# Kernel tuning notes

Measured on AMD Instinct MI355X. Metric: run time of the kernel, lower is better.

The kernel has to match this reference:

```python
import jax, jax.numpy as jnp
import numpy as np

BN_EPS = 1e-5
NEG = -9e15
ALPHA = 0.2  # LeakyReLU slope


def _gat(src, tgt, adj_mask, W, a, num_heads):
    # src: [M, H*D] source features, tgt: [N, H*D], adj_mask: [N, M] (>0 means edge)
    N, M = tgt.shape[0], src.shape[0]
    D = tgt.shape[1] // num_heads
    S = (src @ W.T).reshape(M, num_heads, D)   # W(source)
    T = (tgt @ W.T).reshape(N, num_heads, D)   # W(target)
    # concat([t_i, s_j]) . a[h] == t_i . a[h,:D] + s_j . a[h,D:]
    et = jnp.einsum('nhd,hd->hn', T, a[:, :D])  # [H, N]
    es = jnp.einsum('mhd,hd->hm', S, a[:, D:])  # [H, M]
    e = et[:, :, None] + es[:, None, :]          # [H, N, M]
    e = jnp.where(e >= 0, e, ALPHA * e)          # LeakyReLU
    e = jnp.where(adj_mask[None, :, :] > 0, e, NEG)
    attn = jax.nn.softmax(e, axis=-1)            # over source nodes
    out = jnp.einsum('hnm,mhd->nhd', attn, S)    # [N, H, D]
    return out.reshape(N, num_heads * D)


def _bn_eval(x, gamma, beta):
    # eval-mode BatchNorm1d with running_mean=0, running_var=1
    return x * (gamma / jnp.sqrt(1.0 + BN_EPS)) + beta


def setup_inputs() -> dict:
    key = jax.random.key(0)
    ks = jax.random.split(key, 12)
    N, M, H, HD = 4096, 2048, 8, 256
    D = HD // H
    c_features = jax.random.normal(ks[0], (N, HD), dtype=jnp.float32)
    d_features = jax.random.normal(ks[1], (M, HD), dtype=jnp.float32)
    cd_adj = jax.random.randint(ks[2], (N, M), 0, 2, dtype=jnp.int32)
    sc = 1.0 / np.sqrt(HD)
    c_W = jax.random.normal(ks[3], (HD, HD), dtype=jnp.float32) * sc
    d_W = jax.random.normal(ks[4], (HD, HD), dtype=jnp.float32) * sc
    sa = np.sqrt(2.0 / (H + 2 * D))  # xavier_normal_ for [H, 2D]
    c_a = jax.random.normal(ks[5], (H, 2 * D), dtype=jnp.float32) * sa
    d_a = jax.random.normal(ks[6], (H, 2 * D), dtype=jnp.float32) * sa
    c_bn_gamma = jnp.ones((HD,), dtype=jnp.float32)
    c_bn_beta = jnp.zeros((HD,), dtype=jnp.float32)
    d_bn_gamma = jnp.ones((HD,), dtype=jnp.float32)
    d_bn_beta = jnp.zeros((HD,), dtype=jnp.float32)
    return dict(c_features=c_features, d_features=d_features, cd_adj=cd_adj,
                c_W=c_W, c_a=c_a, d_W=d_W, d_a=d_a,
                c_bn_gamma=c_bn_gamma, c_bn_beta=c_bn_beta,
                d_bn_gamma=d_bn_gamma, d_bn_beta=d_bn_beta)


def reference(c_features, d_features, cd_adj, c_W, c_a, d_W, d_a,
              c_bn_gamma, c_bn_beta, d_bn_gamma, d_bn_beta):
    H = 8
    c_out = _gat(d_features, c_features, cd_adj, c_W, c_a, H)
    d_out = _gat(c_features, d_features, cd_adj.T, d_W, d_a, H)
    c_out = jax.nn.relu(_bn_eval(c_out, c_bn_gamma, c_bn_beta))
    d_out = jax.nn.relu(_bn_eval(d_out, d_bn_gamma, d_bn_beta))
    # dropout is identity in eval mode
    return (c_out, d_out)
```

## Files before the change

### kernel.cpp

```cpp
#include <hip/hip_runtime.h>
#include <hip/hip_bf16.h>

#define L2E 1.4426950408889634f
#define BNF 0.99999500003749969f

typedef __attribute__((ext_vector_type(4))) float f4;
typedef __attribute__((ext_vector_type(4))) float f32x4;
typedef __attribute__((ext_vector_type(4))) int i4;
typedef __attribute__((ext_vector_type(8))) short bfrag;

__device__ __forceinline__ int cvtpk(float lo, float hi) {
  int r;
  asm("v_cvt_pk_bf16_f32 %0, %1, %2" : "=v"(r) : "v"(lo), "v"(hi));
  return r;
}

#define MFMA16(a, b, c) __builtin_amdgcn_mfma_f32_16x16x32_bf16(a, b, c, 0, 0, 0)

__global__ __launch_bounds__(256) void prep1(
    const float* __restrict__ c_feat, const float* __restrict__ d_feat,
    const float* __restrict__ c_W, const float* __restrict__ d_W,
    const float* __restrict__ c_a, const float* __restrict__ d_a,
    const int* __restrict__ adj,
    unsigned* __restrict__ adjP, unsigned* __restrict__ adjPT,
    unsigned short* __restrict__ Xb_c, unsigned short* __restrict__ Xb_d,
    unsigned short* __restrict__ Wb_c, unsigned short* __restrict__ Wb_d,
    float* __restrict__ wa_c, float* __restrict__ wa_d) {
  const int b = blockIdx.x;
  const int t = threadIdx.x;
  if (b < 2048) {
    __shared__ int s[64][65];
    const int m0 = (b & 31) * 64, n0 = (b >> 5) * 64;
#pragma unroll
    for (int i = 0; i < 4; ++i) {
      int idx = t + i * 256;
      int r = idx >> 4, c4 = (idx & 15) * 4;
      i4 v = __builtin_nontemporal_load(
          (const i4*)(adj + (size_t)(n0 + r) * 2048 + m0 + c4));
      s[r][c4 + 0] = v.x; s[r][c4 + 1] = v.y;
      s[r][c4 + 2] = v.z; s[r][c4 + 3] = v.w;
    }
    __syncthreads();
    const int w = t >> 6, l = t & 63;
#pragma unroll 4
    for (int rr = 0; rr < 16; ++rr) {
      int r = w * 16 + rr;
      int n = n0 + r;
      unsigned long long bb = __ballot(s[r][l] != 0);
      if (l == 0) {
        size_t base = ((size_t)(n >> 4) * 64 + (m0 >> 5)) * 16 + (n & 15);
        adjP[base] = (unsigned)bb;
        adjP[base + 16] = (unsigned)(bb >> 32);
      }
    }
#pragma unroll 4
    for (int cc = 0; cc < 16; ++cc) {
      int m = m0 + w * 16 + cc;
      unsigned long long bb = __ballot(s[l][w * 16 + cc] != 0);
      if (l == 0) {
        size_t base = ((size_t)(m >> 4) * 128 + (n0 >> 5)) * 16 + (m & 15);
        adjPT[base] = (unsigned)bb;
        adjPT[base + 16] = (unsigned)(bb >> 32);
      }
    }
  } else if (b < 2880) {
    int idx = (b - 2048) * 256 + t;
    const float* S; unsigned short* D; int tt;
    if (idx < 65536)       { S = d_feat; D = Xb_c; tt = idx; }
    else if (idx < 196608) { S = c_feat; D = Xb_d; tt = idx - 65536; }
    else if (idx < 204800) { S = c_W;    D = Wb_c; tt = idx - 196608; }
    else                   { S = d_W;    D = Wb_d; tt = idx - 204800; }
    int l = tt & 63, kt = (tt >> 6) & 7, tile = tt >> 9;
    int row = tile * 16 + (l & 15);
    int col = kt * 32 + (l >> 4) * 8;
    const float* sp = S + (size_t)row * 256 + col;
    f4 v0 = *(const f4*)sp;
    f4 v1 = *(const f4*)(sp + 4);
    uint4 u;
    u.x = (unsigned)cvtpk(v0.x, v0.y);
    u.y = (unsigned)cvtpk(v0.z, v0.w);
    u.z = (unsigned)cvtpk(v1.x, v1.y);
    u.w = (unsigned)cvtpk(v1.z, v1.w);
    *(uint4*)(D + (size_t)tt * 8) = u;
  } else {
    int idx = (b - 2880) * 256 + t;
    bool cs = idx < 2048;
    int i2 = idx & 2047;
    int h = i2 >> 8, k = i2 & 255;
    const float* W = cs ? c_W : d_W;
    const float* a = cs ? c_a : d_a;
    float s = 0.f;
#pragma unroll 8
    for (int d = 0; d < 32; ++d)
      s = fmaf(a[h * 64 + d], W[(size_t)(h * 32 + d) * 256 + k], s);
    (cs ? wa_c : wa_d)[i2] = s * L2E;
  }
}

__global__ __launch_bounds__(64) void gemm2(
    const unsigned short* __restrict__ Xb_c, const unsigned short* __restrict__ Wb_c,
    const unsigned short* __restrict__ Xb_d, const unsigned short* __restrict__ Wb_d,
    const float* __restrict__ c_a, const float* __restrict__ d_a,
    unsigned short* __restrict__ Sbt_c, unsigned short* __restrict__ Sbt_d,
    float* __restrict__ es2t_c, float* __restrict__ es2t_d,
    const float* __restrict__ c_feat, const float* __restrict__ d_feat,
    const float* __restrict__ wa_c, const float* __restrict__ wa_d,
    float* __restrict__ et2_c, float* __restrict__ et2_d) {
  const int b = blockIdx.x;
  if (b < 768) {
    const bool cs = b < 256;
    const int bb = cs ? b : b - 256;
    const int rt = bb >> 1, half = bb & 1;
    const unsigned short* Xb = cs ? Xb_c : Xb_d;
    const unsigned short* Wb = cs ? Wb_c : Wb_d;
    const float* av = cs ? c_a : d_a;
    unsigned short* Sbt = cs ? Sbt_c : Sbt_d;
    float* es2t = cs ? es2t_c : es2t_d;
    const int Mrows = cs ? 2048 : 4096;
    const int l = threadIdx.x;
    const int g = l >> 4, c16 = l & 15;
    bfrag afr[8];
#pragma unroll
    for (int kt = 0; kt < 8; ++kt)
      afr[kt] = *(const bfrag*)(Xb + ((size_t)(rt * 8 + kt) * 64 + l) * 8);
    float esacc[4] = {};
#pragma unroll
    for (int c8 = 0; c8 < 8; ++c8) {
      const int cht = half * 8 + c8;
      f32x4 acc = {0.f, 0.f, 0.f, 0.f};
#pragma unroll
      for (int kt = 0; kt < 8; ++kt) {
        bfrag wfr = *(const bfrag*)(Wb + ((size_t)(cht * 8 + kt) * 64 + l) * 8);
        acc = MFMA16(afr[kt], wfr, acc);
      }
      const int mtb = rt * 2 + (g >> 1);
      size_t soff = (((size_t)cht * (Mrows >> 3) + mtb) * 16 + c16) * 8 + (g & 1) * 4;
      uint2 u;
      u.x = (unsigned)cvtpk(acc[0], acc[1]);
      u.y = (unsigned)cvtpk(acc[2], acc[3]);
      *(uint2*)(Sbt + soff) = u;
      const int h = cht >> 1, sub = cht & 1;
      const float aw = av[h * 64 + 32 + sub * 16 + c16];
      if (sub == 0) {
#pragma unroll
        for (int i = 0; i < 4; ++i) esacc[i] = acc[i] * aw;
      } else {
#pragma unroll
        for (int i = 0; i < 4; ++i) esacc[i] = fmaf(acc[i], aw, esacc[i]);
#pragma unroll
        for (int i = 0; i < 4; ++i) {
          esacc[i] += __shfl_xor(esacc[i], 1);
          esacc[i] += __shfl_xor(esacc[i], 2);
          esacc[i] += __shfl_xor(esacc[i], 4);
          esacc[i] += __shfl_xor(esacc[i], 8);
        }
        if (c16 == 0) {
          f4 o = {esacc[0] * L2E, esacc[1] * L2E, esacc[2] * L2E, esacc[3] * L2E};
          *(f4*)(es2t + (size_t)h * Mrows + rt * 16 + g * 4) = o;
        }
      }
    }
  } else {
    int idx = (b - 768) * 64 + threadIdx.x;
    bool cs = idx < 32768;
    int i2 = cs ? idx : idx - 32768;
    const float* X = cs ? c_feat : d_feat;
    const float* wa = cs ? wa_c : wa_d;
    float* et2 = cs ? et2_c : et2_d;
    int r = i2 >> 3, h = i2 & 7;
    const float* xp = X + (size_t)r * 256;
    const float* ap = wa + h * 256;
    float s = 0.f;
#pragma unroll 16
    for (int k = 0; k < 256; k += 4) {
      f4 xv = *(const f4*)(xp + k);
      f4 av = *(const f4*)(ap + k);
      s = fmaf(xv.x, av.x, s); s = fmaf(xv.y, av.y, s);
      s = fmaf(xv.z, av.z, s); s = fmaf(xv.w, av.w, s);
    }
    et2[i2] = s;
  }
}

__device__ __forceinline__ bfrag make_pfrag2(float et, f4 e0, f4 e1,
                                             unsigned bits) {
  float xv[8] = {e0.x, e0.y, e0.z, e0.w, e1.x, e1.y, e1.z, e1.w};
  float p[8];
#pragma unroll
  for (int e = 0; e < 8; ++e) {
    float x = et + xv[e];
    x = fmaxf(x, 0.2f * x);
    float pe = __builtin_amdgcn_exp2f(x);
    p[e] = ((bits >> e) & 1u) ? pe : 0.f;
  }
  union { bfrag v; int i[4]; } u;
#pragma unroll
  for (int e = 0; e < 4; ++e) u.i[e] = cvtpk(p[2 * e], p[2 * e + 1]);
  return u.v;
}

template <int FINAL, int SWZ, int CHT>
__global__ __launch_bounds__(256) void fused_attn(
    const float* __restrict__ et2_c, const float* __restrict__ es2t_c,
    const unsigned* __restrict__ adjP, const unsigned short* __restrict__ Sbt_c,
    float* __restrict__ pnum_c, float* __restrict__ pden_c,
    const float* __restrict__ et2_d, const float* __restrict__ es2t_d,
    const unsigned* __restrict__ adjPT, const unsigned short* __restrict__ Sbt_d,
    float* __restrict__ pnum_d, float* __restrict__ pden_d,
    float* __restrict__ out,
    const float* __restrict__ gc, const float* __restrict__ bc,
    const float* __restrict__ gd, const float* __restrict__ bd,
    int NBC, int CH_C, int CH_D) {
  const int b = blockIdx.x;
  bool cs; int chunk, tile;
  if (SWZ) {
    const int r = b & 7;
    if (r < 4) { cs = true;  chunk = r >> 1; tile = (b >> 3) + (r & 1) * 128; }
    else       { cs = false; chunk = r - 4;  tile = b >> 3; }
  } else {
    cs = b < NBC;
    const int bb = cs ? b : b - NBC;
    tile = cs ? (bb & 255) : (bb & 127);
    chunk = cs ? (bb >> 8) : (bb >> 7);
  }
  const int n0 = tile * 16;
  const int M = cs ? 2048 : 4096;
  const int ROWS = cs ? 4096 : 2048;
  const int CH = CHT ? CHT : (cs ? CH_C : CH_D);
  const float* et2 = cs ? et2_c : et2_d;
  const float* es2t = cs ? es2t_c : es2t_d;
  const unsigned* adjPk = cs ? adjP : adjPT;
  const unsigned short* Sbt = cs ? Sbt_c : Sbt_d;
  float* pnum = cs ? pnum_c : pnum_d;
  float* pden = cs ? pden_c : pden_d;
  const float* bng = cs ? gc : gd;
  const float* bnb = cs ? bc : bd;
  float* outp = cs ? out : out + (size_t)4096 * 256;

  const int mstart = chunk * CH;
  const int mend = mstart + CH;
  const int Mw = M >> 5;
  const int tid = threadIdx.x;
  const int w = tid >> 6, l = tid & 63;
  const int g = l >> 4, c16 = l & 15;
  const int hA = w * 2, hB = w * 2 + 1;
  const int row = n0 + c16;
  const float etA = et2[row * 8 + hA];
  const float etB = et2[row * 8 + hB];
  const int Mt16 = M * 16;
  const int lane_off = g * 128 + c16 * 8;
  const unsigned short* pA0 = Sbt + (size_t)(hA * 2) * Mt16 + lane_off;
  const unsigned short* pA1 = pA0 + Mt16;
  const unsigned short* pB0 = Sbt + (size_t)(hB * 2) * Mt16 + lane_off;
  const unsigned short* pB1 = pB0 + Mt16;
  const unsigned* adjt = adjPk + (size_t)tile * Mw * 16 + c16;
  const float* esArow = es2t + (size_t)hA * M;
  const float* esBrow = es2t + (size_t)hB * M;
  f32x4 accA0 = {0.f, 0.f, 0.f, 0.f}, accA1 = accA0, denA = accA0;
  f32x4 accB0 = accA0, accB1 = accA0, denB = accA0;
  union { bfrag v; int i[4]; } uo;
#pragma unroll
  for (int e = 0; e < 4; ++e) uo.i[e] = 0x3F803F80;
  const bfrag ones = uo.v;

  auto body = [&](int m0) {
    const unsigned w0 = adjt[(m0 >> 5) * 16];
    const unsigned w1 = adjt[(m0 >> 5) * 16 + 16];
    const int moa = m0 + g * 8;
    const int i8 = (m0 >> 3) * 128;
    f4 eA0 = *(const f4*)(esArow + moa);
    f4 eA1 = *(const f4*)(esArow + moa + 4);
    f4 eB0 = *(const f4*)(esBrow + moa);
    f4 eB1 = *(const f4*)(esBrow + moa + 4);
    f4 fA0 = *(const f4*)(esArow + moa + 32);
    f4 fA1 = *(const f4*)(esArow + moa + 36);
    f4 fB0 = *(const f4*)(esBrow + moa + 32);
    f4 fB1 = *(const f4*)(esBrow + moa + 36);
    bfrag bA0a = *(const bfrag*)(pA0 + i8);
    bfrag bA1a = *(const bfrag*)(pA1 + i8);
    bfrag bB0a = *(const bfrag*)(pB0 + i8);
    bfrag bB1a = *(const bfrag*)(pB1 + i8);
    bfrag bA0b = *(const bfrag*)(pA0 + i8 + 512);
    bfrag bA1b = *(const bfrag*)(pA1 + i8 + 512);
    bfrag bB0b = *(const bfrag*)(pB0 + i8 + 512);
    bfrag bB1b = *(const bfrag*)(pB1 + i8 + 512);
    const unsigned bits0 = (w0 >> (g * 8)) & 0xffu;
    const unsigned bits1 = (w1 >> (g * 8)) & 0xffu;
    bfrag aA = make_pfrag2(etA, eA0, eA1, bits0);
    bfrag aB = make_pfrag2(etB, eB0, eB1, bits0);
    __builtin_amdgcn_s_setprio(1);
    accA0 = MFMA16(aA, bA0a, accA0);
    accA1 = MFMA16(aA, bA1a, accA1);
    denA  = MFMA16(aA, ones, denA);
    accB0 = MFMA16(aB, bB0a, accB0);
    accB1 = MFMA16(aB, bB1a, accB1);
    denB  = MFMA16(aB, ones, denB);
    __builtin_amdgcn_s_setprio(0);
    bfrag cA = make_pfrag2(etA, fA0, fA1, bits1);
    bfrag cB = make_pfrag2(etB, fB0, fB1, bits1);
    __builtin_amdgcn_s_setprio(1);
    accA0 = MFMA16(cA, bA0b, accA0);
    accA1 = MFMA16(cA, bA1b, accA1);
    denA  = MFMA16(cA, ones, denA);
    accB0 = MFMA16(cB, bB0b, accB0);
    accB1 = MFMA16(cB, bB1b, accB1);
    denB  = MFMA16(cB, ones, denB);
    __builtin_amdgcn_s_setprio(0);
  };

  if (CHT) {
#pragma unroll 1
    for (int mm = 0; mm < CHT; mm += 512) {
#pragma unroll
      for (int it = 0; it < 8; ++it)
        body(mstart + mm + it * 64);
    }
  } else {
    for (int m0 = mstart; m0 < mend; m0 += 64)
      body(m0);
  }

#define EPILOGUE(acc0, acc1, den, h)                                          \
  {                                                                           \
    const int c0 = (h) * 32 + c16, c1 = (h) * 32 + 16 + c16;                  \
    if (FINAL) {                                                              \
      const float g0 = bng[c0] * BNF, b0 = bnb[c0];                           \
      const float g1 = bng[c1] * BNF, b1 = bnb[c1];                           \
      _Pragma("unroll") for (int i = 0; i < 4; ++i) {                         \
        float rs = 1.f / fmaxf(den[i], 1e-30f);                               \
        float* op = outp + (size_t)(n0 + g * 4 + i) * 256;                    \
        op[c0] = fmaxf(fmaf(acc0[i] * rs, g0, b0), 0.f);                      \
        op[c1] = fmaxf(fmaf(acc1[i] * rs, g1, b1), 0.f);                      \
      }                                                                       \
    } else {                                                                  \
      _Pragma("unroll") for (int i = 0; i < 4; ++i) {                         \
        size_t rr = (size_t)chunk * ROWS + n0 + g * 4 + i;                    \
        pnum[rr * 256 + c0] = acc0[i];                                        \
        pnum[rr * 256 + c1] = acc1[i];                                        \
        if (c16 == 0) pden[rr * 8 + (h)] = den[i];                            \
      }                                                                       \
    }                                                                         \
  }
  EPILOGUE(accA0, accA1, denA, hA)
  EPILOGUE(accB0, accB1, denB, hB)
#undef EPILOGUE
}

__global__ __launch_bounds__(256) void finalize_k(
    const float* __restrict__ pnum_c, const float* __restrict__ pden_c,
    const float* __restrict__ pnum_d, const float* __restrict__ pden_d,
    float* __restrict__ out,
    const float* __restrict__ gc, const float* __restrict__ bc,
    const float* __restrict__ gd, const float* __restrict__ bd,
    int cc_c, int cc_d) {
  const int b = blockIdx.x;
  const bool cs = b < 1024;
  const int idx = (cs ? b : b - 1024) * 256 + threadIdx.x;
  const int rows = cs ? 4096 : 2048;
  const int cc = cs ? cc_c : cc_d;
  const float* pnum = cs ? pnum_c : pnum_d;
  const float* pden = cs ? pden_c : pden_d;
  const float* bng = cs ? gc : gd;
  const float* bnb = cs ? bc : bd;
  float* outp = cs ? out : out + (size_t)4096 * 256;
  int r = idx >> 6, c4 = (idx & 63) * 4;
  int h = c4 >> 5;
  f4 num = {0.f, 0.f, 0.f, 0.f};
  float den = 0.f;
  for (int c = 0; c < cc; ++c) {
    size_t rr = (size_t)c * rows + r;
    num += __builtin_nontemporal_load((const f4*)(pnum + rr * 256 + c4));
    den += __builtin_nontemporal_load(pden + rr * 8 + h);
  }
  float rs = 1.f / fmaxf(den, 1e-30f);
  f4 gm = *(const f4*)(bng + c4);
  f4 bb = *(const f4*)(bnb + c4);
  f4 o;
  o.x = fmaxf(fmaf(num.x * rs, gm.x * BNF, bb.x), 0.f);
  o.y = fmaxf(fmaf(num.y * rs, gm.y * BNF, bb.y), 0.f);
  o.z = fmaxf(fmaf(num.z * rs, gm.z * BNF, bb.z), 0.f);
  o.w = fmaxf(fmaf(num.w * rs, gm.w * BNF, bb.w), 0.f);
  *(f4*)(outp + (size_t)r * 256 + c4) = o;
}

extern "C" void kernel_launch(void* const* d_in, const int* in_sizes, int n_in,
                              void* d_out, int out_size, void* d_ws, size_t ws_size,
                              hipStream_t stream) {
  const float* c_feat = (const float*)d_in[0];
  const float* d_feat = (const float*)d_in[1];
  const int*   adj    = (const int*)d_in[2];
  const float* c_W    = (const float*)d_in[3];
  const float* c_a    = (const float*)d_in[4];
  const float* d_W    = (const float*)d_in[5];
  const float* d_a    = (const float*)d_in[6];
  const float* c_bn_g = (const float*)d_in[7];
  const float* c_bn_b = (const float*)d_in[8];
  const float* d_bn_g = (const float*)d_in[9];
  const float* d_bn_b = (const float*)d_in[10];
  float* out = (float*)d_out;

  char* w = (char*)d_ws;
  size_t off = 0;
  auto take = [&](size_t bytes) -> char* {
    char* p = w + off;
    off += (bytes + 255) & ~(size_t)255;
    return p;
  };
  unsigned short* Sbt_c = (unsigned short*)take(256 * 2048 * 2);
  unsigned short* Sbt_d = (unsigned short*)take(256 * 4096 * 2);
  unsigned short* Xb_c  = (unsigned short*)take(2048 * 256 * 2);
  unsigned short* Xb_d  = (unsigned short*)take(4096 * 256 * 2);
  unsigned short* Wb_c  = (unsigned short*)take(256 * 256 * 2);
  unsigned short* Wb_d  = (unsigned short*)take(256 * 256 * 2);
  float* et2_c  = (float*)take(4096 * 8 * 4);
  float* es2t_c = (float*)take(8 * 2048 * 4);
  float* et2_d  = (float*)take(2048 * 8 * 4);
  float* es2t_d = (float*)take(8 * 4096 * 4);
  float* wa_c   = (float*)take(8 * 256 * 4);
  float* wa_d   = (float*)take(8 * 256 * 4);
  unsigned* adjP  = (unsigned*)take(4096 * 64 * 4);
  unsigned* adjPT = (unsigned*)take(2048 * 128 * 4);

  const size_t base = off;
  const size_t PC = (size_t)4096 * 256 * 4, PD = (size_t)2048 * 256 * 4;
  const size_t DC = 4096 * 8 * 4, DD = 2048 * 8 * 4;
  auto need = [&](int a, int b2) -> size_t {
    return base + (size_t)a * (PC + DC) + (size_t)b2 * (PD + DD) + 4096;
  };
  int ccc = 0, ccd = 0;
  if (ws_size >= need(2, 4))      { ccc = 2; ccd = 4; }
  else if (ws_size >= need(2, 2)) { ccc = 2; ccd = 2; }

  float* pden_c = nullptr; float* pden_d = nullptr;
  float* pnum_c = nullptr; float* pnum_d = nullptr;
  if (ccc) {
    pden_c = (float*)take((size_t)ccc * DC);
    pden_d = (float*)take((size_t)ccd * DD);
    pnum_c = (float*)take((size_t)ccc * PC);
    pnum_d = (float*)take((size_t)ccd * PD);
  }

  dim3 blk(256);
  prep1<<<2896, blk, 0, stream>>>(c_feat, d_feat, c_W, d_W, c_a, d_a, adj,
                                  adjP, adjPT, Xb_c, Xb_d, Wb_c, Wb_d,
                                  wa_c, wa_d);
  gemm2<<<1536, dim3(64), 0, stream>>>(Xb_c, Wb_c, Xb_d, Wb_d, c_a, d_a,
                                       Sbt_c, Sbt_d, es2t_c, es2t_d,
                                       c_feat, d_feat, wa_c, wa_d,
                                       et2_c, et2_d);

  if (ccc == 2 && ccd == 4) {
    fused_attn<0, 1, 1024><<<1024, blk, 0, stream>>>(
        et2_c, es2t_c, adjP, Sbt_c, pnum_c, pden_c,
        et2_d, es2t_d, adjPT, Sbt_d, pnum_d, pden_d,
        nullptr, c_bn_g, c_bn_b, d_bn_g, d_bn_b,
        512, 1024, 1024);
    finalize_k<<<1536, blk, 0, stream>>>(pnum_c, pden_c, pnum_d, pden_d, out,
                                         c_bn_g, c_bn_b, d_bn_g, d_bn_b, ccc, ccd);
  } else if (ccc) {
    fused_attn<0, 0, 0><<<256 * ccc + 128 * ccd, blk, 0, stream>>>(
        et2_c, es2t_c, adjP, Sbt_c, pnum_c, pden_c,
        et2_d, es2t_d, adjPT, Sbt_d, pnum_d, pden_d,
        nullptr, c_bn_g, c_bn_b, d_bn_g, d_bn_b,
        256 * ccc, 2048 / ccc, 4096 / ccd);
    finalize_k<<<1536, blk, 0, stream>>>(pnum_c, pden_c, pnum_d, pden_d, out,
                                         c_bn_g, c_bn_b, d_bn_g, d_bn_b, ccc, ccd);
  } else {
    fused_attn<1, 0, 0><<<384, blk, 0, stream>>>(
        et2_c, es2t_c, adjP, Sbt_c, nullptr, nullptr,
        et2_d, es2t_d, adjPT, Sbt_d, nullptr, nullptr,
        out, c_bn_g, c_bn_b, d_bn_g, d_bn_b, 256, 2048, 4096);
  }
}
```

Baseline: 73.93 us.

## Move adjacency bit-packing into the GEMM kernel and shrink the prep kernel

Measured after the change: 76.42 us. 1.03x slower.

```diff
diff --git a/kernel.cpp b/kernel.cpp
--- a/kernel.cpp
+++ b/kernel.cpp
@@ -17,54 +17,17 @@
 
 #define MFMA16(a, b, c) __builtin_amdgcn_mfma_f32_16x16x32_bf16(a, b, c, 0, 0, 0)
 
-__global__ __launch_bounds__(256) void prep1(
+__global__ __launch_bounds__(256) void conv_wa(
     const float* __restrict__ c_feat, const float* __restrict__ d_feat,
     const float* __restrict__ c_W, const float* __restrict__ d_W,
     const float* __restrict__ c_a, const float* __restrict__ d_a,
-    const int* __restrict__ adj,
-    unsigned* __restrict__ adjP, unsigned* __restrict__ adjPT,
     unsigned short* __restrict__ Xb_c, unsigned short* __restrict__ Xb_d,
     unsigned short* __restrict__ Wb_c, unsigned short* __restrict__ Wb_d,
     float* __restrict__ wa_c, float* __restrict__ wa_d) {
   const int b = blockIdx.x;
   const int t = threadIdx.x;
-  if (b < 2048) {
-    __shared__ int s[64][65];
-    const int m0 = (b & 31) * 64, n0 = (b >> 5) * 64;
-#pragma unroll
-    for (int i = 0; i < 4; ++i) {
-      int idx = t + i * 256;
-      int r = idx >> 4, c4 = (idx & 15) * 4;
-      i4 v = __builtin_nontemporal_load(
-          (const i4*)(adj + (size_t)(n0 + r) * 2048 + m0 + c4));
-      s[r][c4 + 0] = v.x; s[r][c4 + 1] = v.y;
-      s[r][c4 + 2] = v.z; s[r][c4 + 3] = v.w;
-    }
-    __syncthreads();
-    const int w = t >> 6, l = t & 63;
-#pragma unroll 4
-    for (int rr = 0; rr < 16; ++rr) {
-      int r = w * 16 + rr;
-      int n = n0 + r;
-      unsigned long long bb = __ballot(s[r][l] != 0);
-      if (l == 0) {
-        size_t base = ((size_t)(n >> 4) * 64 + (m0 >> 5)) * 16 + (n & 15);
-        adjP[base] = (unsigned)bb;
-        adjP[base + 16] = (unsigned)(bb >> 32);
-      }
-    }
-#pragma unroll 4
-    for (int cc = 0; cc < 16; ++cc) {
-      int m = m0 + w * 16 + cc;
-      unsigned long long bb = __ballot(s[l][w * 16 + cc] != 0);
-      if (l == 0) {
-        size_t base = ((size_t)(m >> 4) * 128 + (n0 >> 5)) * 16 + (m & 15);
-        adjPT[base] = (unsigned)bb;
-        adjPT[base + 16] = (unsigned)(bb >> 32);
-      }
-    }
-  } else if (b < 2880) {
-    int idx = (b - 2048) * 256 + t;
+  if (b < 832) {
+    int idx = b * 256 + t;
     const float* S; unsigned short* D; int tt;
     if (idx < 65536)       { S = d_feat; D = Xb_c; tt = idx; }
     else if (idx < 196608) { S = c_feat; D = Xb_d; tt = idx - 65536; }
@@ -83,7 +46,7 @@
     u.w = (unsigned)cvtpk(v1.z, v1.w);
     *(uint4*)(D + (size_t)tt * 8) = u;
   } else {
-    int idx = (b - 2880) * 256 + t;
+    int idx = (b - 832) * 256 + t;
     bool cs = idx < 2048;
     int i2 = idx & 2047;
     int h = i2 >> 8, k = i2 & 255;
@@ -97,7 +60,7 @@
   }
 }
 
-__global__ __launch_bounds__(64) void gemm2(
+__global__ __launch_bounds__(256) void mid_k(
     const unsigned short* __restrict__ Xb_c, const unsigned short* __restrict__ Wb_c,
     const unsigned short* __restrict__ Xb_d, const unsigned short* __restrict__ Wb_d,
     const float* __restrict__ c_a, const float* __restrict__ d_a,
@@ -105,11 +68,15 @@
     float* __restrict__ es2t_c, float* __restrict__ es2t_d,
     const float* __restrict__ c_feat, const float* __restrict__ d_feat,
     const float* __restrict__ wa_c, const float* __restrict__ wa_d,
-    float* __restrict__ et2_c, float* __restrict__ et2_d) {
+    float* __restrict__ et2_c, float* __restrict__ et2_d,
+    const int* __restrict__ adj,
+    unsigned* __restrict__ adjP, unsigned* __restrict__ adjPT) {
   const int b = blockIdx.x;
-  if (b < 768) {
-    const bool cs = b < 256;
-    const int bb = cs ? b : b - 256;
+  const int t = threadIdx.x;
+  if (b < 192) {
+    const int vb = b * 4 + (t >> 6);
+    const bool cs = vb < 256;
+    const int bb = cs ? vb : vb - 256;
     const int rt = bb >> 1, half = bb & 1;
     const unsigned short* Xb = cs ? Xb_c : Xb_d;
     const unsigned short* Wb = cs ? Wb_c : Wb_d;
@@ -117,7 +84,7 @@
     unsigned short* Sbt = cs ? Sbt_c : Sbt_d;
     float* es2t = cs ? es2t_c : es2t_d;
     const int Mrows = cs ? 2048 : 4096;
-    const int l = threadIdx.x;
+    const int l = t & 63;
     const int g = l >> 4, c16 = l & 15;
     bfrag afr[8];
 #pragma unroll
@@ -160,8 +127,9 @@
         }
       }
     }
-  } else {
-    int idx = (b - 768) * 64 + threadIdx.x;
+  } else if (b < 384) {
+    const int vb = (b - 192) * 4 + (t >> 6);
+    int idx = vb * 64 + (t & 63);
     bool cs = idx < 32768;
     int i2 = cs ? idx : idx - 32768;
     const float* X = cs ? c_feat : d_feat;
@@ -179,6 +147,42 @@
       s = fmaf(xv.z, av.z, s); s = fmaf(xv.w, av.w, s);
     }
     et2[i2] = s;
+  } else {
+    __shared__ int s[64][65];
+    const int bb = b - 384;
+    const int m0 = (bb & 31) * 64, n0 = (bb >> 5) * 64;
+#pragma unroll
+    for (int i = 0; i < 4; ++i) {
+      int idx = t + i * 256;
+      int r = idx >> 4, c4 = (idx & 15) * 4;
+      i4 v = __builtin_nontemporal_load(
+          (const i4*)(adj + (size_t)(n0 + r) * 2048 + m0 + c4));
+      s[r][c4 + 0] = v.x; s[r][c4 + 1] = v.y;
+      s[r][c4 + 2] = v.z; s[r][c4 + 3] = v.w;
+    }
+    __syncthreads();
+    const int w = t >> 6, l = t & 63;
+#pragma unroll 4
+    for (int rr = 0; rr < 16; ++rr) {
+      int r = w * 16 + rr;
+      int n = n0 + r;
+      unsigned long long bb2 = __ballot(s[r][l] != 0);
+      if (l == 0) {
+        size_t base = ((size_t)(n >> 4) * 64 + (m0 >> 5)) * 16 + (n & 15);
+        adjP[base] = (unsigned)bb2;
+        adjP[base + 16] = (unsigned)(bb2 >> 32);
+      }
+    }
+#pragma unroll 4
+    for (int cc = 0; cc < 16; ++cc) {
+      int m = m0 + w * 16 + cc;
+      unsigned long long bb2 = __ballot(s[l][w * 16 + cc] != 0);
+      if (l == 0) {
+        size_t base = ((size_t)(m >> 4) * 128 + (n0 >> 5)) * 16 + (m & 15);
+        adjPT[base] = (unsigned)bb2;
+        adjPT[base + 16] = (unsigned)(bb2 >> 32);
+      }
+    }
   }
 }
 
@@ -441,13 +445,12 @@
   }
 
   dim3 blk(256);
-  prep1<<<2896, blk, 0, stream>>>(c_feat, d_feat, c_W, d_W, c_a, d_a, adj,
-                                  adjP, adjPT, Xb_c, Xb_d, Wb_c, Wb_d,
-                                  wa_c, wa_d);
-  gemm2<<<1536, dim3(64), 0, stream>>>(Xb_c, Wb_c, Xb_d, Wb_d, c_a, d_a,
-                                       Sbt_c, Sbt_d, es2t_c, es2t_d,
-                                       c_feat, d_feat, wa_c, wa_d,
-                                       et2_c, et2_d);
+  conv_wa<<<848, blk, 0, stream>>>(c_feat, d_feat, c_W, d_W, c_a, d_a,
+                                   Xb_c, Xb_d, Wb_c, Wb_d, wa_c, wa_d);
+  mid_k<<<2432, blk, 0, stream>>>(Xb_c, Wb_c, Xb_d, Wb_d, c_a, d_a,
+                                  Sbt_c, Sbt_d, es2t_c, es2t_d,
+                                  c_feat, d_feat, wa_c, wa_d,
+                                  et2_c, et2_d, adj, adjP, adjPT);
 
   if (ccc == 2 && ccd == 4) {
     fused_attn<0, 1, 1024><<<1024, blk, 0, stream>>>(
```
